# Optimization experiments

Hardware: AMD Instinct MI355X
Metric: run time of the kernel (lower is better)

## Reference

```python
import jax, jax.numpy as jnp
import numpy as np

N_HEAD = 16
SCALE = True
NEG = 10000.0


def setup_inputs() -> dict:
    key = jax.random.key(0)
    ks = jax.random.split(key, 5)
    B, S, D = 4, 1024, 1024
    x = jax.random.normal(ks[0], (B, S, D), dtype=jnp.float32)
    # GPT-2 Conv1D weights: W has shape [in, out], init ~N(0, 0.02)
    w_attn = jax.random.normal(ks[1], (D, 3 * D), dtype=jnp.float32) * 0.02
    b_attn = jnp.zeros((3 * D,), dtype=jnp.float32)
    w_proj = jax.random.normal(ks[2], (D, D), dtype=jnp.float32) * 0.02
    b_proj = jnp.zeros((D,), dtype=jnp.float32)
    return {"x": x, "w_attn": w_attn, "b_attn": b_attn,
            "w_proj": w_proj, "b_proj": b_proj}


def reference(x, w_attn, b_attn, w_proj, b_proj):
    B, S, D = x.shape
    H = N_HEAD
    hd = D // H
    # c_attn: Conv1D == x @ W + b
    qkv = jnp.einsum('bsd,de->bse', x, w_attn) + b_attn
    q, k, v = jnp.split(qkv, 3, axis=-1)
    # split heads -> [B, H, S, hd]
    q = q.reshape(B, S, H, hd).transpose(0, 2, 1, 3)
    k = k.reshape(B, S, H, hd).transpose(0, 2, 1, 3)
    v = v.reshape(B, S, H, hd).transpose(0, 2, 1, 3)
    # scores [B, H, S, S]
    w = jnp.einsum('bhqd,bhkd->bhqk', q, k)
    if SCALE:
        w = w / jnp.sqrt(jnp.float32(hd))
    # multiplicative causal mask: w*b - 10000*(1-b)
    bmask = jnp.tril(jnp.ones((S, S), dtype=w.dtype))[None, None]
    w = w * bmask - NEG * (1.0 - bmask)
    w = jax.nn.softmax(w, axis=-1)
    # attn_pdrop = 0 -> dropout is identity
    a = jnp.einsum('bhqk,bhkd->bhqd', w, v)
    # merge heads
    a = a.transpose(0, 2, 1, 3).reshape(B, S, D)
    # c_proj; resid_pdrop = 0
    out = jnp.einsum('bsd,de->bse', a, w_proj) + b_proj
    return out
```

## Files before the change

kernel.cpp:

```cpp
#include <hip/hip_runtime.h>
#include <hip/hip_bf16.h>


typedef __bf16 bf16x8 __attribute__((ext_vector_type(8)));
typedef float f32x4 __attribute__((ext_vector_type(4)));

__device__ __forceinline__ void load_lds16(const void* g, void* l) {
  __builtin_amdgcn_global_load_lds(
      (const __attribute__((address_space(1))) void*)g,
      (__attribute__((address_space(3))) void*)l, 16, 0, 0);
}

__global__ __launch_bounds__(256) void prep(
    const float* __restrict__ x, const float* __restrict__ w_attn,
    const float* __restrict__ w_proj, __bf16* __restrict__ Xb,
    __bf16* __restrict__ WT_attn, __bf16* __restrict__ WT_proj) {
  __shared__ __bf16 tile[32][33];
  const int blk = blockIdx.x;
  const int tid = threadIdx.x;
  if (blk < 4096) {
    const float* W;
    __bf16* WT;
    int n0, k0, N;
    if (blk < 3072) {
      W = w_attn; WT = WT_attn; N = 3072;
      n0 = (blk % 96) * 32; k0 = (blk / 96) * 32;
    } else {
      W = w_proj; WT = WT_proj; N = 1024;
      const int t = blk - 3072;
      n0 = (t & 31) * 32; k0 = (t >> 5) * 32;
    }
    const int tx = tid & 31, ty = tid >> 5;
#pragma unroll
    for (int j = 0; j < 32; j += 8)
      tile[ty + j][tx] = (__bf16)W[(size_t)(k0 + ty + j) * N + n0 + tx];
    __syncthreads();
#pragma unroll
    for (int j = 0; j < 32; j += 8)
      WT[(size_t)(n0 + ty + j) * 1024 + k0 + tx] = tile[tx][ty + j];
  } else {
    const size_t i = (size_t)(blk - 4096) * 4096 + tid * 16;
    const float4* xp = (const float4*)(x + i);
    float4 a = xp[0], b = xp[1], c = xp[2], d = xp[3];
    bf16x8 o0, o1;
    o0[0] = (__bf16)a.x; o0[1] = (__bf16)a.y; o0[2] = (__bf16)a.z; o0[3] = (__bf16)a.w;
    o0[4] = (__bf16)b.x; o0[5] = (__bf16)b.y; o0[6] = (__bf16)b.z; o0[7] = (__bf16)b.w;
    o1[0] = (__bf16)c.x; o1[1] = (__bf16)c.y; o1[2] = (__bf16)c.z; o1[3] = (__bf16)c.w;
    o1[4] = (__bf16)d.x; o1[5] = (__bf16)d.y; o1[6] = (__bf16)d.z; o1[7] = (__bf16)d.w;
    *(bf16x8*)(Xb + i) = o0;
    *(bf16x8*)(Xb + i + 8) = o1;
  }
}

__global__ __launch_bounds__(256) void transpose_v(
    const __bf16* __restrict__ Vr, __bf16* __restrict__ VT) {
  const int lane = threadIdx.x & 63, wave = threadIdx.x >> 6;
  const int bh = blockIdx.x >> 4;
  const int kb = (blockIdx.x & 15) * 64;
  const int b = bh >> 4, h = bh & 15;
  const __bf16* src =
      Vr + (size_t)(b * 1024 + kb + lane) * 1024 + h * 64 + wave * 16;
  bf16x8 v0 = *(const bf16x8*)src;
  bf16x8 v1 = *(const bf16x8*)(src + 8);
  __bf16* dst = VT + ((size_t)bh * 64 + wave * 16) * 1024 + kb + lane;
#pragma unroll
  for (int i = 0; i < 8; ++i) {
    dst[(size_t)i * 1024] = v0[i];
    dst[(size_t)(i + 8) * 1024] = v1[i];
  }
}

#define GEMM_CORE(A_, BT_, K_)                                                   \
  __shared__ __bf16 sA[128 * 64];                                                \
  __shared__ __bf16 sB[128 * 64];                                                \
  const int tid = threadIdx.x;                                                   \
  const int lane = tid & 63;                                                     \
  const int wave = tid >> 6;                                                     \
  const int waveM = wave >> 1, waveN = wave & 1;                                 \
  const int quad = lane >> 4;                                                    \
  const int l16 = lane & 15;                                                     \
  const int rowBase = blockIdx.y * 128;                                          \
  const int colBase = blockIdx.x * 128;                                          \
  const int sr = lane >> 3;                                                      \
  const int ss = lane & 7;                                                       \
  const int gcs = ss ^ sr;                                                       \
  const int swl = l16 & 7;                                                       \
  f32x4 acc[4][4] = {};                                                          \
  for (int k0 = 0; k0 < K_; k0 += 64) {                                          \
    __syncthreads();                                                             \
    _Pragma("unroll") for (int i = 0; i < 4; ++i) {                              \
      const int rb = wave * 32 + i * 8;                                          \
      load_lds16(&A_[(size_t)(rowBase + rb + sr) * K_ + k0 + gcs * 8],           \
                 &sA[rb * 64]);                                                  \
      load_lds16(&BT_[(size_t)(colBase + rb + sr) * K_ + k0 + gcs * 8],          \
                 &sB[rb * 64]);                                                  \
    }                                                                            \
    __syncthreads();                                                             \
    bf16x8 af0[4], af1[4], bf0[4], bf1[4];                                       \
    _Pragma("unroll") for (int mt = 0; mt < 4; ++mt) {                           \
      const int row = waveM * 64 + mt * 16 + l16;                                \
      af0[mt] = *(const bf16x8*)(&sA[row * 64 + ((quad ^ swl) << 3)]);           \
      af1[mt] = *(const bf16x8*)(&sA[row * 64 + (((quad + 4) ^ swl) << 3)]);     \
    }                                                                            \
    _Pragma("unroll") for (int nt = 0; nt < 4; ++nt) {                           \
      const int row = waveN * 64 + nt * 16 + l16;                                \
      bf0[nt] = *(const bf16x8*)(&sB[row * 64 + ((quad ^ swl) << 3)]);           \
      bf1[nt] = *(const bf16x8*)(&sB[row * 64 + (((quad + 4) ^ swl) << 3)]);     \
    }                                                                            \
    _Pragma("unroll") for (int mt = 0; mt < 4; ++mt)                             \
    _Pragma("unroll") for (int nt = 0; nt < 4; ++nt) {                           \
      acc[mt][nt] = __builtin_amdgcn_mfma_f32_16x16x32_bf16(                     \
          af0[mt], bf0[nt], acc[mt][nt], 0, 0, 0);                               \
      acc[mt][nt] = __builtin_amdgcn_mfma_f32_16x16x32_bf16(                     \
          af1[mt], bf1[nt], acc[mt][nt], 0, 0, 0);                               \
    }                                                                            \
  }

__global__ __launch_bounds__(256) void gemm_qkv(
    const __bf16* __restrict__ A, const __bf16* __restrict__ BT,
    const float* __restrict__ bias, __bf16* __restrict__ Qp,
    __bf16* __restrict__ Kp, __bf16* __restrict__ Vr) {
  GEMM_CORE(A, BT, 1024)
  const int seg = colBase >> 10;
#pragma unroll
  for (int mt = 0; mt < 4; ++mt) {
    const int row0 = rowBase + waveM * 64 + mt * 16 + quad * 4;
#pragma unroll
    for (int nt = 0; nt < 4; ++nt) {
      const int col = colBase + waveN * 64 + nt * 16 + l16;
      const float bv = bias[col];
      const int cc = col & 1023;
#pragma unroll
      for (int r = 0; r < 4; ++r) {
        const int row = row0 + r;
        const float v = acc[mt][nt][r] + bv;
        if (seg == 2) {
          Vr[(size_t)row * 1024 + cc] = (__bf16)v;
        } else {
          const int bh = ((row >> 10) << 4) + (cc >> 6);
          __bf16* dst = (seg == 0) ? Qp : Kp;
          dst[((size_t)bh << 16) + (size_t)(row & 1023) * 64 + (cc & 63)] =
              (__bf16)v;
        }
      }
    }
  }
}

__global__ __launch_bounds__(256) void gemm_out(
    const __bf16* __restrict__ A, const __bf16* __restrict__ BT,
    const float* __restrict__ bias, float* __restrict__ C) {
  GEMM_CORE(A, BT, 1024)
#pragma unroll
  for (int mt = 0; mt < 4; ++mt) {
    const int row = rowBase + waveM * 64 + mt * 16 + quad * 4;
#pragma unroll
    for (int nt = 0; nt < 4; ++nt) {
      const int col = colBase + waveN * 64 + nt * 16 + l16;
      const float bv = bias[col];
#pragma unroll
      for (int r = 0; r < 4; ++r)
        C[(size_t)(row + r) * 1024 + col] = acc[mt][nt][r] + bv;
    }
  }
}

__global__ __launch_bounds__(256) void attn_mfma(
    const __bf16* __restrict__ Qp, const __bf16* __restrict__ Kp,
    const __bf16* __restrict__ VT, __bf16* __restrict__ Aout) {
  __shared__ __bf16 sK[128 * 64];
  __shared__ __bf16 sV[64 * 128];
  __shared__ __bf16 sP[4 * 16 * 128];

  const int tid = threadIdx.x;
  const int lane = tid & 63;
  const int wave = tid >> 6;
  const int quad = lane >> 4;
  const int l16 = lane & 15;
  const int swq = l16 & 7;

  const int bh = blockIdx.x >> 3;
  const int pr = blockIdx.x & 7;
  const int b = bh >> 4, h = bh & 15;
  const int qbA = pr * 64, qbB = (15 - pr) * 64;
  const int ktA_max = pr >> 1, ktB_max = (15 - pr) >> 1;

  const __bf16* Qb = Qp + ((size_t)bh << 16);
  const __bf16* Kb = Kp + ((size_t)bh << 16);
  const __bf16* VTb = VT + (size_t)bh * 64 * 1024;

  bf16x8 qA0A, qA1A, qA0B, qA1B;
  {
    const __bf16* qr = Qb + (size_t)(qbA + wave * 16 + l16) * 64 + quad * 8;
    qA0A = *(const bf16x8*)qr;
    qA1A = *(const bf16x8*)(qr + 32);
    qr = Qb + (size_t)(qbB + wave * 16 + l16) * 64 + quad * 8;
    qA0B = *(const bf16x8*)qr;
    qA1B = *(const bf16x8*)(qr + 32);
  }

  f32x4 OA[4] = {}, OB[4] = {};
  float psA[4] = {0.f, 0.f, 0.f, 0.f}, psB[4] = {0.f, 0.f, 0.f, 0.f};
  __bf16* pw = sP + wave * 2048;

  for (int kt = 0; kt <= ktB_max; ++kt) {
    const int kb = kt * 128;
    __syncthreads();

#pragma unroll
    for (int i = 0; i < 4; ++i) {
      const int rb = wave * 32 + i * 8;
      load_lds16(Kb + (size_t)(kb + rb + (lane >> 3)) * 64 +
                     (((lane & 7) ^ ((lane >> 3) & 7)) << 3),
                 &sK[rb * 64]);
    }
#pragma unroll
    for (int i = 0; i < 4; ++i) {
      const int db = wave * 16 + i * 4;
      const int d = db + (lane >> 4);
      load_lds16(VTb + (size_t)d * 1024 + kb + (((lane & 15) ^ (d & 7)) << 3),
                 &sV[db * 128]);
    }
    __syncthreads();

    {
      float sc[8][4];
#pragma unroll
      for (int n = 0; n < 8; ++n) {
        const int key = n * 16 + l16;
        bf16x8 kB0 = *(const bf16x8*)(&sK[key * 64 + ((quad ^ swq) << 3)]);
        bf16x8 kB1 = *(const bf16x8*)(&sK[key * 64 + (((quad + 4) ^ swq) << 3)]);
        f32x4 c = {};
        c = __builtin_amdgcn_mfma_f32_16x16x32_bf16(qA0B, kB0, c, 0, 0, 0);
        c = __builtin_amdgcn_mfma_f32_16x16x32_bf16(qA1B, kB1, c, 0, 0, 0);
#pragma unroll
        for (int r = 0; r < 4; ++r) sc[n][r] = c[r] * 0.125f;
      }
      if (kt == ktB_max) {
#pragma unroll
        for (int n = 0; n < 8; ++n) {
          const int kg = kb + n * 16 + l16;
#pragma unroll
          for (int r = 0; r < 4; ++r)
            if (kg > qbB + wave * 16 + quad * 4 + r) sc[n][r] = -1.0e30f;
        }
      }
#pragma unroll
      for (int n = 0; n < 8; ++n)
#pragma unroll
        for (int r = 0; r < 4; ++r) {
          float p = __expf(fminf(sc[n][r], 60.0f));
          sc[n][r] = p;
          psB[r] += p;
        }
      {
        const int kb8 = l16 >> 3, lo = l16 & 7;
#pragma unroll
        for (int n = 0; n < 8; ++n) {
          const int chunk = n * 2 + kb8;
#pragma unroll
          for (int r = 0; r < 4; ++r) {
            const int q = quad * 4 + r;
            pw[q * 128 + ((chunk ^ (q & 7)) << 3) + lo] = (__bf16)sc[n][r];
          }
        }
      }
#pragma unroll
      for (int cc = 0; cc < 4; ++cc) {
        bf16x8 pA = *(const bf16x8*)(&pw[l16 * 128 + (((cc * 4 + quad) ^ swq) << 3)]);
#pragma unroll
        for (int nt = 0; nt < 4; ++nt) {
          bf16x8 vB = *(const bf16x8*)(&sV[(nt * 16 + l16) * 128 +
                                           (((cc * 4 + quad) ^ swq) << 3)]);
          OB[nt] = __builtin_amdgcn_mfma_f32_16x16x32_bf16(pA, vB, OB[nt], 0, 0, 0);
        }
      }
    }

    if (kt <= ktA_max) {
      float sc[8][4];
#pragma unroll
      for (int n = 0; n < 8; ++n) {
        const int key = n * 16 + l16;
        bf16x8 kB0 = *(const bf16x8*)(&sK[key * 64 + ((quad ^ swq) << 3)]);
        bf16x8 kB1 = *(const bf16x8*)(&sK[key * 64 + (((quad + 4) ^ swq) << 3)]);
        f32x4 c = {};
        c = __builtin_amdgcn_mfma_f32_16x16x32_bf16(qA0A, kB0, c, 0, 0, 0);
        c = __builtin_amdgcn_mfma_f32_16x16x32_bf16(qA1A, kB1, c, 0, 0, 0);
#pragma unroll
        for (int r = 0; r < 4; ++r) sc[n][r] = c[r] * 0.125f;
      }
      if (kt == ktA_max) {
#pragma unroll
        for (int n = 0; n < 8; ++n) {
          const int kg = kb + n * 16 + l16;
#pragma unroll
          for (int r = 0; r < 4; ++r)
            if (kg > qbA + wave * 16 + quad * 4 + r) sc[n][r] = -1.0e30f;
        }
      }
#pragma unroll
      for (int n = 0; n < 8; ++n)
#pragma unroll
        for (int r = 0; r < 4; ++r) {
          float p = __expf(fminf(sc[n][r], 60.0f));
          sc[n][r] = p;
          psA[r] += p;
        }
      {
        const int kb8 = l16 >> 3, lo = l16 & 7;
#pragma unroll
        for (int n = 0; n < 8; ++n) {
          const int chunk = n * 2 + kb8;
#pragma unroll
          for (int r = 0; r < 4; ++r) {
            const int q = quad * 4 + r;
            pw[q * 128 + ((chunk ^ (q & 7)) << 3) + lo] = (__bf16)sc[n][r];
          }
        }
      }
#pragma unroll
      for (int cc = 0; cc < 4; ++cc) {
        bf16x8 pA = *(const bf16x8*)(&pw[l16 * 128 + (((cc * 4 + quad) ^ swq) << 3)]);
#pragma unroll
        for (int nt = 0; nt < 4; ++nt) {
          bf16x8 vB = *(const bf16x8*)(&sV[(nt * 16 + l16) * 128 +
                                           (((cc * 4 + quad) ^ swq) << 3)]);
          OA[nt] = __builtin_amdgcn_mfma_f32_16x16x32_bf16(pA, vB, OA[nt], 0, 0, 0);
        }
      }
    }
  }

  float invA[4], invB[4];
#pragma unroll
  for (int r = 0; r < 4; ++r) {
    float pa = psA[r], pb = psB[r];
    pa += __shfl_xor(pa, 1); pb += __shfl_xor(pb, 1);
    pa += __shfl_xor(pa, 2); pb += __shfl_xor(pb, 2);
    pa += __shfl_xor(pa, 4); pb += __shfl_xor(pb, 4);
    pa += __shfl_xor(pa, 8); pb += __shfl_xor(pb, 8);
    invA[r] = 1.0f / pa;
    invB[r] = 1.0f / pb;
  }
#pragma unroll
  for (int nt = 0; nt < 4; ++nt) {
#pragma unroll
    for (int r = 0; r < 4; ++r) {
      const int qA = qbA + wave * 16 + quad * 4 + r;
      const int qB = qbB + wave * 16 + quad * 4 + r;
      Aout[((size_t)b * 1024 + qA) * 1024 + h * 64 + nt * 16 + l16] =
          (__bf16)(OA[nt][r] * invA[r]);
      Aout[((size_t)b * 1024 + qB) * 1024 + h * 64 + nt * 16 + l16] =
          (__bf16)(OB[nt][r] * invB[r]);
    }
  }
}

extern "C" void kernel_launch(void* const* d_in, const int* in_sizes, int n_in,
                              void* d_out, int out_size, void* d_ws,
                              size_t ws_size, hipStream_t stream) {
  const float* x      = (const float*)d_in[0];
  const float* w_attn = (const float*)d_in[1];
  const float* b_attn = (const float*)d_in[2];
  const float* w_proj = (const float*)d_in[3];
  const float* b_proj = (const float*)d_in[4];
  float* out = (float*)d_out;

  char* ws = (char*)d_ws;
  __bf16* WT_attn = (__bf16*)(ws);
  __bf16* WT_proj = (__bf16*)(ws + 6291456);
  __bf16* Xb      = (__bf16*)(ws + 8388608);
  __bf16* Qp      = (__bf16*)(ws + 16777216);
  __bf16* Kp      = (__bf16*)(ws + 25165824);
  __bf16* Vr      = (__bf16*)(ws + 33554432);
  __bf16* Aattn   = (__bf16*)(ws + 41943040);
  __bf16* VT      = Xb;

  prep<<<5120, 256, 0, stream>>>(x, w_attn, w_proj, Xb, WT_attn, WT_proj);
  gemm_qkv<<<dim3(24, 32), 256, 0, stream>>>(Xb, WT_attn, b_attn, Qp, Kp, Vr);
  transpose_v<<<1024, 256, 0, stream>>>(Vr, VT);
  attn_mfma<<<512, 256, 0, stream>>>(Qp, Kp, VT, Aattn);
  gemm_out<<<dim3(8, 32), 256, 0, stream>>>(Aattn, WT_proj, b_proj, out);
}
```

Measured before the change: 186.1 us.

## Shrink GEMM K-tile, double-buffer K in attention, and reuse V fragments

The GEMM core now stages 32-wide K slices with a new XOR swizzle instead of 64-wide ones. This halves shared memory per block but doubles the number of barrier-separated iterations. The attention kernel double-buffers K tiles so the next tile's load overlaps the current QK^T, and it computes both query blocks' scores from one read of the K fragments. V fragments are held in registers and reused for the second P·V, and launch bounds request 2 blocks per CU. In exchange, register pressure rises from holding vBreg and both score sets, and the extra syncs and smaller GEMM tiles may cut throughput.

After: 206.2 us. 10.8% more time.

```diff
diff --git a/kernel.cpp b/kernel.cpp
--- a/kernel.cpp
+++ b/kernel.cpp
@@ -71,49 +71,42 @@
 }
 
 #define GEMM_CORE(A_, BT_, K_)                                                   \
-  __shared__ __bf16 sA[128 * 64];                                                \
-  __shared__ __bf16 sB[128 * 64];                                                \
-  const int tid = threadIdx.x;                                                   \
-  const int lane = tid & 63;                                                     \
-  const int wave = tid >> 6;                                                     \
-  const int waveM = wave >> 1, waveN = wave & 1;                                 \
-  const int quad = lane >> 4;                                                    \
-  const int l16 = lane & 15;                                                     \
-  const int rowBase = blockIdx.y * 128;                                          \
-  const int colBase = blockIdx.x * 128;                                          \
-  const int sr = lane >> 3;                                                      \
-  const int ss = lane & 7;                                                       \
-  const int gcs = ss ^ sr;                                                       \
-  const int swl = l16 & 7;                                                       \
-  f32x4 acc[4][4] = {};                                                          \
-  for (int k0 = 0; k0 < K_; k0 += 64) {                                          \
-    __syncthreads();                                                             \
-    _Pragma("unroll") for (int i = 0; i < 4; ++i) {                              \
-      const int rb = wave * 32 + i * 8;                                          \
-      load_lds16(&A_[(size_t)(rowBase + rb + sr) * K_ + k0 + gcs * 8],           \
-                 &sA[rb * 64]);                                                  \
-      load_lds16(&BT_[(size_t)(colBase + rb + sr) * K_ + k0 + gcs * 8],          \
-                 &sB[rb * 64]);                                                  \
-    }                                                                            \
-    __syncthreads();                                                             \
-    bf16x8 af0[4], af1[4], bf0[4], bf1[4];                                       \
-    _Pragma("unroll") for (int mt = 0; mt < 4; ++mt) {                           \
-      const int row = waveM * 64 + mt * 16 + l16;                                \
-      af0[mt] = *(const bf16x8*)(&sA[row * 64 + ((quad ^ swl) << 3)]);           \
-      af1[mt] = *(const bf16x8*)(&sA[row * 64 + (((quad + 4) ^ swl) << 3)]);     \
-    }                                                                            \
-    _Pragma("unroll") for (int nt = 0; nt < 4; ++nt) {                           \
-      const int row = waveN * 64 + nt * 16 + l16;                                \
-      bf0[nt] = *(const bf16x8*)(&sB[row * 64 + ((quad ^ swl) << 3)]);           \
-      bf1[nt] = *(const bf16x8*)(&sB[row * 64 + (((quad + 4) ^ swl) << 3)]);     \
-    }                                                                            \
-    _Pragma("unroll") for (int mt = 0; mt < 4; ++mt)                             \
-    _Pragma("unroll") for (int nt = 0; nt < 4; ++nt) {                           \
-      acc[mt][nt] = __builtin_amdgcn_mfma_f32_16x16x32_bf16(                     \
-          af0[mt], bf0[nt], acc[mt][nt], 0, 0, 0);                               \
-      acc[mt][nt] = __builtin_amdgcn_mfma_f32_16x16x32_bf16(                     \
-          af1[mt], bf1[nt], acc[mt][nt], 0, 0, 0);                               \
-    }                                                                            \
+  __shared__ __bf16 sA[128 * 32];                                               \
+  __shared__ __bf16 sB[128 * 32];                                               \
+  const int tid = threadIdx.x;                                                  \
+  const int lane = tid & 63;                                                    \
+  const int wave = tid >> 6;                                                    \
+  const int waveM = wave >> 1, waveN = wave & 1;                                \
+  const int quad = lane >> 4;                                                   \
+  const int l16 = lane & 15;                                                    \
+  const int rowBase = blockIdx.y * 128;                                         \
+  const int colBase = blockIdx.x * 128;                                         \
+  const int rIn = lane >> 2;                                                    \
+  const int sIn = lane & 3;                                                     \
+  const int gc = sIn ^ (rIn & 3) ^ ((rIn >> 2) & 3);                            \
+  const int readSlot = quad ^ (l16 & 3) ^ ((l16 >> 2) & 3);                     \
+  f32x4 acc[4][4] = {};                                                         \
+  for (int k0 = 0; k0 < K_; k0 += 32) {                                         \
+    __syncthreads();                                                            \
+    _Pragma("unroll") for (int j = 0; j < 2; ++j) {                             \
+      const int rb = wave * 32 + j * 16;                                        \
+      load_lds16(&A_[(size_t)(rowBase + rb + rIn) * K_ + k0 + gc * 8],          \
+                 &sA[rb * 32]);                                                 \
+      load_lds16(&BT_[(size_t)(colBase + rb + rIn) * K_ + k0 + gc * 8],         \
+                 &sB[rb * 32]);                                                 \
+    }                                                                           \
+    __syncthreads();                                                            \
+    bf16x8 af[4], bfr[4];                                                       \
+    _Pragma("unroll") for (int mt = 0; mt < 4; ++mt)                            \
+      af[mt] = *(const bf16x8*)(&sA[(waveM * 64 + mt * 16 + l16) * 32 +         \
+                                    readSlot * 8]);                             \
+    _Pragma("unroll") for (int nt = 0; nt < 4; ++nt)                            \
+      bfr[nt] = *(const bf16x8*)(&sB[(waveN * 64 + nt * 16 + l16) * 32 +        \
+                                     readSlot * 8]);                            \
+    _Pragma("unroll") for (int mt = 0; mt < 4; ++mt)                            \
+    _Pragma("unroll") for (int nt = 0; nt < 4; ++nt)                            \
+      acc[mt][nt] = __builtin_amdgcn_mfma_f32_16x16x32_bf16(                    \
+          af[mt], bfr[nt], acc[mt][nt], 0, 0, 0);                               \
   }
 
 __global__ __launch_bounds__(256) void gemm_qkv(
@@ -165,12 +158,12 @@
   }
 }
 
-__global__ __launch_bounds__(256) void attn_mfma(
+__global__ __launch_bounds__(256, 2) void attn_mfma(
     const __bf16* __restrict__ Qp, const __bf16* __restrict__ Kp,
     const __bf16* __restrict__ VT, __bf16* __restrict__ Aout) {
-  __shared__ __bf16 sK[128 * 64];
+  __shared__ __bf16 sK[2][128 * 64];
   __shared__ __bf16 sV[64 * 128];
-  __shared__ __bf16 sP[4 * 16 * 128];
+  __shared__ __bf16 sP[4][2048];
 
   const int tid = threadIdx.x;
   const int lane = tid & 63;
@@ -201,133 +194,116 @@
 
   f32x4 OA[4] = {}, OB[4] = {};
   float psA[4] = {0.f, 0.f, 0.f, 0.f}, psB[4] = {0.f, 0.f, 0.f, 0.f};
-  __bf16* pw = sP + wave * 2048;
+  __bf16* pw = sP[wave];
+
+  const int krow = lane >> 3, kslot = lane & 7;
+  const int vrow = lane >> 4, vslot = lane & 15;
+
+#pragma unroll
+  for (int i = 0; i < 4; ++i) {
+    const int rb = wave * 32 + i * 8;
+    load_lds16(Kb + (size_t)(rb + krow) * 64 + ((kslot ^ krow) << 3),
+               &sK[0][rb * 64]);
+  }
 
   for (int kt = 0; kt <= ktB_max; ++kt) {
+    const int cur = kt & 1;
     const int kb = kt * 128;
     __syncthreads();
 
-#pragma unroll
-    for (int i = 0; i < 4; ++i) {
-      const int rb = wave * 32 + i * 8;
-      load_lds16(Kb + (size_t)(kb + rb + (lane >> 3)) * 64 +
-                     (((lane & 7) ^ ((lane >> 3) & 7)) << 3),
-                 &sK[rb * 64]);
+    if (kt < ktB_max) {
+#pragma unroll
+      for (int i = 0; i < 4; ++i) {
+        const int rb = wave * 32 + i * 8;
+        load_lds16(Kb + (size_t)(kb + 128 + rb + krow) * 64 + ((kslot ^ krow) << 3),
+                   &sK[cur ^ 1][rb * 64]);
+      }
     }
 #pragma unroll
     for (int i = 0; i < 4; ++i) {
       const int db = wave * 16 + i * 4;
-      const int d = db + (lane >> 4);
-      load_lds16(VTb + (size_t)d * 1024 + kb + (((lane & 15) ^ (d & 7)) << 3),
+      const int d = db + vrow;
+      load_lds16(VTb + (size_t)d * 1024 + kb + ((vslot ^ (d & 7)) << 3),
                  &sV[db * 128]);
     }
+
+    const bool aAct = (kt <= ktA_max);
+    const __bf16* kbuf = sK[cur];
+
+    f32x4 cB[8], cA[8];
+#pragma unroll
+    for (int n = 0; n < 8; ++n) {
+      const int key = n * 16 + l16;
+      bf16x8 k0 = *(const bf16x8*)(&kbuf[key * 64 + ((quad ^ swq) << 3)]);
+      bf16x8 k1 = *(const bf16x8*)(&kbuf[key * 64 + (((quad + 4) ^ swq) << 3)]);
+      f32x4 c = {};
+      c = __builtin_amdgcn_mfma_f32_16x16x32_bf16(qA0B, k0, c, 0, 0, 0);
+      c = __builtin_amdgcn_mfma_f32_16x16x32_bf16(qA1B, k1, c, 0, 0, 0);
+      cB[n] = c;
+      if (aAct) {
+        f32x4 d = {};
+        d = __builtin_amdgcn_mfma_f32_16x16x32_bf16(qA0A, k0, d, 0, 0, 0);
+        d = __builtin_amdgcn_mfma_f32_16x16x32_bf16(qA1A, k1, d, 0, 0, 0);
+        cA[n] = d;
+      }
+    }
+
+    {
+      const int kb8 = l16 >> 3, lo = l16 & 7;
+#pragma unroll
+      for (int n = 0; n < 8; ++n) {
+        const int kg = kb + n * 16 + l16;
+        const int chunk = n * 2 + kb8;
+#pragma unroll
+        for (int r = 0; r < 4; ++r) {
+          float s = cB[n][r] * 0.125f;
+          if (kt == ktB_max && kg > qbB + wave * 16 + quad * 4 + r) s = -1.0e30f;
+          const float p = __expf(fminf(s, 60.0f));
+          psB[r] += p;
+          const int q = quad * 4 + r;
+          pw[q * 128 + ((chunk ^ (q & 7)) << 3) + lo] = (__bf16)p;
+        }
+      }
+    }
+
     __syncthreads();
 
-    {
-      float sc[8][4];
+    bf16x8 vBreg[4][4];
+#pragma unroll
+    for (int cc = 0; cc < 4; ++cc) {
+      bf16x8 pA = *(const bf16x8*)(&pw[l16 * 128 + (((cc * 4 + quad) ^ swq) << 3)]);
+#pragma unroll
+      for (int nt = 0; nt < 4; ++nt) {
+        vBreg[cc][nt] = *(const bf16x8*)(&sV[(nt * 16 + l16) * 128 +
+                                             (((cc * 4 + quad) ^ swq) << 3)]);
+        OB[nt] = __builtin_amdgcn_mfma_f32_16x16x32_bf16(pA, vBreg[cc][nt],
+                                                         OB[nt], 0, 0, 0);
+      }
+    }
+
+    if (aAct) {
+      const int kb8 = l16 >> 3, lo = l16 & 7;
 #pragma unroll
       for (int n = 0; n < 8; ++n) {
-        const int key = n * 16 + l16;
-        bf16x8 kB0 = *(const bf16x8*)(&sK[key * 64 + ((quad ^ swq) << 3)]);
-        bf16x8 kB1 = *(const bf16x8*)(&sK[key * 64 + (((quad + 4) ^ swq) << 3)]);
-        f32x4 c = {};
-        c = __builtin_amdgcn_mfma_f32_16x16x32_bf16(qA0B, kB0, c, 0, 0, 0);
-        c = __builtin_amdgcn_mfma_f32_16x16x32_bf16(qA1B, kB1, c, 0, 0, 0);
-#pragma unroll
-        for (int r = 0; r < 4; ++r) sc[n][r] = c[r] * 0.125f;
-      }
-      if (kt == ktB_max) {
-#pragma unroll
-        for (int n = 0; n < 8; ++n) {
-          const int kg = kb + n * 16 + l16;
-#pragma unroll
-          for (int r = 0; r < 4; ++r)
-            if (kg > qbB + wave * 16 + quad * 4 + r) sc[n][r] = -1.0e30f;
-        }
-      }
-#pragma unroll
-      for (int n = 0; n < 8; ++n)
+        const int kg = kb + n * 16 + l16;
+        const int chunk = n * 2 + kb8;
 #pragma unroll
         for (int r = 0; r < 4; ++r) {
-          float p = __expf(fminf(sc[n][r], 60.0f));
-          sc[n][r] = p;
-          psB[r] += p;
-        }
-      {
-        const int kb8 = l16 >> 3, lo = l16 & 7;
-#pragma unroll
-        for (int n = 0; n < 8; ++n) {
-          const int chunk = n * 2 + kb8;
-#pragma unroll
-          for (int r = 0; r < 4; ++r) {
-            const int q = quad * 4 + r;
-            pw[q * 128 + ((chunk ^ (q & 7)) << 3) + lo] = (__bf16)sc[n][r];
-          }
+          float s = cA[n][r] * 0.125f;
+          if (kt == ktA_max && kg > qbA + wave * 16 + quad * 4 + r) s = -1.0e30f;
+          const float p = __expf(fminf(s, 60.0f));
+          psA[r] += p;
+          const int q = quad * 4 + r;
+          pw[q * 128 + ((chunk ^ (q & 7)) << 3) + lo] = (__bf16)p;
         }
       }
 #pragma unroll
       for (int cc = 0; cc < 4; ++cc) {
         bf16x8 pA = *(const bf16x8*)(&pw[l16 * 128 + (((cc * 4 + quad) ^ swq) << 3)]);
 #pragma unroll
-        for (int nt = 0; nt < 4; ++nt) {
-          bf16x8 vB = *(const bf16x8*)(&sV[(nt * 16 + l16) * 128 +
-                                           (((cc * 4 + quad) ^ swq) << 3)]);
-          OB[nt] = __builtin_amdgcn_mfma_f32_16x16x32_bf16(pA, vB, OB[nt], 0, 0, 0);
-        }
-      }
-    }
-
-    if (kt <= ktA_max) {
-      float sc[8][4];
-#pragma unroll
-      for (int n = 0; n < 8; ++n) {
-        const int key = n * 16 + l16;
-        bf16x8 kB0 = *(const bf16x8*)(&sK[key * 64 + ((quad ^ swq) << 3)]);
-        bf16x8 kB1 = *(const bf16x8*)(&sK[key * 64 + (((quad + 4) ^ swq) << 3)]);
-        f32x4 c = {};
-        c = __builtin_amdgcn_mfma_f32_16x16x32_bf16(qA0A, kB0, c, 0, 0, 0);
-        c = __builtin_amdgcn_mfma_f32_16x16x32_bf16(qA1A, kB1, c, 0, 0, 0);
-#pragma unroll
-        for (int r = 0; r < 4; ++r) sc[n][r] = c[r] * 0.125f;
-      }
-      if (kt == ktA_max) {
-#pragma unroll
-        for (int n = 0; n < 8; ++n) {
-          const int kg = kb + n * 16 + l16;
-#pragma unroll
-          for (int r = 0; r < 4; ++r)
-            if (kg > qbA + wave * 16 + quad * 4 + r) sc[n][r] = -1.0e30f;
-        }
-      }
-#pragma unroll
-      for (int n = 0; n < 8; ++n)
-#pragma unroll
-        for (int r = 0; r < 4; ++r) {
-          float p = __expf(fminf(sc[n][r], 60.0f));
-          sc[n][r] = p;
-          psA[r] += p;
-        }
-      {
-        const int kb8 = l16 >> 3, lo = l16 & 7;
-#pragma unroll
-        for (int n = 0; n < 8; ++n) {
-          const int chunk = n * 2 + kb8;
-#pragma unroll
-          for (int r = 0; r < 4; ++r) {
-            const int q = quad * 4 + r;
-            pw[q * 128 + ((chunk ^ (q & 7)) << 3) + lo] = (__bf16)sc[n][r];
-          }
-        }
-      }
-#pragma unroll
-      for (int cc = 0; cc < 4; ++cc) {
-        bf16x8 pA = *(const bf16x8*)(&pw[l16 * 128 + (((cc * 4 + quad) ^ swq) << 3)]);
-#pragma unroll
-        for (int nt = 0; nt < 4; ++nt) {
-          bf16x8 vB = *(const bf16x8*)(&sV[(nt * 16 + l16) * 128 +
-                                           (((cc * 4 + quad) ^ swq) << 3)]);
-          OA[nt] = __builtin_amdgcn_mfma_f32_16x16x32_bf16(pA, vB, OA[nt], 0, 0, 0);
-        }
+        for (int nt = 0; nt < 4; ++nt)
+          OA[nt] = __builtin_amdgcn_mfma_f32_16x16x32_bf16(pA, vBreg[cc][nt],
+                                                           OA[nt], 0, 0, 0);
       }
     }
   }
```
